# Kernel optimization log

Hardware: AMD Instinct MI355X
Metric: run time of the kernel (lower is better)

## Reference

```python
import jax, jax.numpy as jnp
import numpy as np

N_HEADS = 16
NEG_INF = -1e30


def apply_rope(x, cos, sin):
    # x: (B, T, H, D); cos/sin: (>=T, D//2)
    d = x.shape[-1]
    x1, x2 = x[..., : d // 2], x[..., d // 2 :]
    c = cos[: x.shape[1], :][None, :, None, :]  # (1, T, 1, D//2)
    s = sin[: x.shape[1], :][None, :, None, :]
    return jnp.concatenate([x1 * c - x2 * s, x2 * c + x1 * s], axis=-1)


def setup_inputs() -> dict:
    key = jax.random.key(0)
    k1, k2, k3, k4, k5 = jax.random.split(key, 5)
    B, T, D = 4, 2048, 2048
    hd = D // N_HEADS
    scale = 0.02
    return {
        "x": jax.random.normal(k1, (B, T, D), dtype=jnp.float32),
        "cos": jax.random.uniform(k2, (T, hd // 2), dtype=jnp.float32),
        "sin": jax.random.uniform(k3, (T, hd // 2), dtype=jnp.float32),
        "W_qkv": jax.random.normal(k4, (3 * D, D), dtype=jnp.float32) * scale,
        "W_out": jax.random.normal(k5, (D, D), dtype=jnp.float32) * scale,
    }


def reference(x, cos, sin, W_qkv, W_out):
    B, T, D = x.shape
    H = N_HEADS
    hd = D // H
    # fused QKV projection (torch Linear: y = x @ W.T)
    qkv = jnp.einsum("btd,ed->bte", x, W_qkv).reshape(B, T, 3, H, hd)
    q, k, v = qkv[:, :, 0], qkv[:, :, 1], qkv[:, :, 2]
    q = apply_rope(q, cos, sin)
    k = apply_rope(k, cos, sin)
    # causal SDPA, scale = 1/sqrt(head_dim)
    scores = jnp.einsum("bthd,bshd->bhts", q, k) / jnp.sqrt(jnp.asarray(hd, x.dtype))
    causal = jnp.tril(jnp.ones((T, T), dtype=bool))  # (T, T)
    scores = jnp.where(causal[None, None, :, :], scores, NEG_INF)
    attn = jax.nn.softmax(scores, axis=-1)
    out = jnp.einsum("bhts,bshd->bthd", attn, v).reshape(B, T, D)
    return jnp.einsum("btd,ed->bte", out, W_out)
```

## Files before the change

### kernel.cpp

```cpp
#include <hip/hip_runtime.h>
#include <hip/hip_bf16.h>
#include <stdint.h>

#define TDIM 2048
#define DDIM 2048
#define BDIM 4
#define HDIM 16
#define HD   128
#define E3   6144
#define KDIM 2048

typedef unsigned short u16;
typedef __bf16 bf16x8 __attribute__((ext_vector_type(8)));
typedef float  f32x4  __attribute__((ext_vector_type(4)));

__device__ __forceinline__ u16 f2bf(float f) {
  union { float f; uint32_t u; } x; x.f = f;
  uint32_t r = x.u + 0x7fffu + ((x.u >> 16) & 1u);
  return (u16)(r >> 16);
}
__device__ __forceinline__ float bf2f(u16 u) {
  union { uint32_t u; float f; } x; x.u = ((uint32_t)u) << 16;
  return x.f;
}

__device__ __forceinline__ void load16(const void* g, void* l) {
  __builtin_amdgcn_global_load_lds(
      (const __attribute__((address_space(1))) void*)g,
      (__attribute__((address_space(3))) void*)l, 16, 0, 0);
}

__global__ void cvt_kernel(const float* __restrict__ in, u16* __restrict__ out, int n) {
  int i = (blockIdx.x * 256 + threadIdx.x) * 4;
  if (i >= n) return;
  float4 v = *(const float4*)(in + i);
  ushort4 o;
  o.x = f2bf(v.x); o.y = f2bf(v.y); o.z = f2bf(v.z); o.w = f2bf(v.w);
  *(ushort4*)(out + i) = o;
}

template <int MODE>
__global__ __launch_bounds__(256) void gemm_bt(
    const u16* __restrict__ A, const u16* __restrict__ Bm,
    u16* __restrict__ qkOut, u16* __restrict__ vtOut, float* __restrict__ fOut) {
  __shared__ __align__(16) u16 As[128 * 64];
  __shared__ __align__(16) u16 Bs[128 * 64];
  const int tid = threadIdx.x;
  const int bn = blockIdx.x, bm = blockIdx.y;
  const int w = tid >> 6, lane = tid & 63;
  const int wr = w >> 1, wc = w & 1;
  const int lrow = lane & 15, lgrp = lane >> 4;

  f32x4 acc[4][4];
#pragma unroll
  for (int m = 0; m < 4; ++m)
#pragma unroll
    for (int n = 0; n < 4; ++n) {
      acc[m][n][0] = 0.f; acc[m][n][1] = 0.f; acc[m][n][2] = 0.f; acc[m][n][3] = 0.f;
    }

  const size_t aRow = (size_t)bm * 128;
  const size_t bRow = (size_t)bn * 128;

  for (int kt = 0; kt < KDIM / 64; ++kt) {
    const int kb = kt * 64;
#pragma unroll
    for (int is = 0; is < 4; ++is) {
      int u = is * 256 + tid;
      int r = u >> 3, blk = u & 7;
      load16(A + (aRow + r) * KDIM + kb + ((blk ^ (r & 7)) * 8),
             (char*)As + (size_t)u * 16);
    }
#pragma unroll
    for (int is = 0; is < 4; ++is) {
      int u = is * 256 + tid;
      int r = u >> 3, blk = u & 7;
      load16(Bm + (bRow + r) * KDIM + kb + ((blk ^ (r & 7)) * 8),
             (char*)Bs + (size_t)u * 16);
    }
    __syncthreads();

#pragma unroll
    for (int kk = 0; kk < 2; ++kk) {
      bf16x8 af[4], bfr[4];
#pragma unroll
      for (int m = 0; m < 4; ++m) {
        int row = wr * 64 + m * 16 + lrow;
        af[m] = *(const bf16x8*)(As + row * 64 + (((kk * 4 + lgrp) ^ (row & 7)) * 8));
      }
#pragma unroll
      for (int n = 0; n < 4; ++n) {
        int row = wc * 64 + n * 16 + lrow;
        bfr[n] = *(const bf16x8*)(Bs + row * 64 + (((kk * 4 + lgrp) ^ (row & 7)) * 8));
      }
#pragma unroll
      for (int m = 0; m < 4; ++m)
#pragma unroll
        for (int n = 0; n < 4; ++n)
          acc[m][n] = __builtin_amdgcn_mfma_f32_16x16x32_bf16(af[m], bfr[n], acc[m][n], 0, 0, 0);
    }
    __syncthreads();
  }

  const int col_base = bn * 128 + wc * 64;
  const int row_base = bm * 128 + wr * 64;
#pragma unroll
  for (int m = 0; m < 4; ++m) {
    int row0 = row_base + m * 16 + lgrp * 4;
#pragma unroll
    for (int n = 0; n < 4; ++n) {
      int col = col_base + n * 16 + lrow;
      if (MODE == 0) {
        if (bn < 32) {
#pragma unroll
          for (int i = 0; i < 4; ++i)
            qkOut[(size_t)(row0 + i) * 4096 + col] = f2bf(acc[m][n][i]);
        } else {
          int e = col - 4096;
          int hh = e >> 7, d = e & 127;
          int bb = row0 >> 11, t0 = row0 & 2047;
          ushort4 pk;
          pk.x = f2bf(acc[m][n][0]); pk.y = f2bf(acc[m][n][1]);
          pk.z = f2bf(acc[m][n][2]); pk.w = f2bf(acc[m][n][3]);
          *(ushort4*)(vtOut + ((size_t)(bb * HDIM + hh) * HD + d) * TDIM + t0) = pk;
        }
      } else {
#pragma unroll
        for (int i = 0; i < 4; ++i)
          fOut[(size_t)(row0 + i) * DDIM + col] = acc[m][n][i];
      }
    }
  }
}

__global__ void rope_kernel(u16* __restrict__ qkbuf,
                            const float* __restrict__ cosb, const float* __restrict__ sinb) {
  int gid = blockIdx.x * 256 + threadIdx.x;
  int d4 = gid & 15;
  int h = (gid >> 4) & 15;
  int which = (gid >> 8) & 1;
  int row = gid >> 9;
  int t = row & 2047;
  u16* base = qkbuf + (size_t)row * 4096 + which * 2048 + h * HD + d4 * 4;
  ushort4 u1 = *(ushort4*)base;
  ushort4 u2 = *(ushort4*)(base + 64);
  float4 c = *(const float4*)(cosb + (size_t)t * 64 + d4 * 4);
  float4 s = *(const float4*)(sinb + (size_t)t * 64 + d4 * 4);
  float x1[4] = {bf2f(u1.x), bf2f(u1.y), bf2f(u1.z), bf2f(u1.w)};
  float x2[4] = {bf2f(u2.x), bf2f(u2.y), bf2f(u2.z), bf2f(u2.w)};
  float cc[4] = {c.x, c.y, c.z, c.w};
  float ss[4] = {s.x, s.y, s.z, s.w};
  ushort4 o1, o2;
  o1.x = f2bf(x1[0]*cc[0] - x2[0]*ss[0]); o2.x = f2bf(x2[0]*cc[0] + x1[0]*ss[0]);
  o1.y = f2bf(x1[1]*cc[1] - x2[1]*ss[1]); o2.y = f2bf(x2[1]*cc[1] + x1[1]*ss[1]);
  o1.z = f2bf(x1[2]*cc[2] - x2[2]*ss[2]); o2.z = f2bf(x2[2]*cc[2] + x1[2]*ss[2]);
  o1.w = f2bf(x1[3]*cc[3] - x2[3]*ss[3]); o2.w = f2bf(x2[3]*cc[3] + x1[3]*ss[3]);
  *(ushort4*)base = o1;
  *(ushort4*)(base + 64) = o2;
}

__global__ __launch_bounds__(256) void attn_kernel(const u16* __restrict__ qkbuf,
                                                   const u16* __restrict__ vtbuf,
                                                   u16* __restrict__ ao) {
  __shared__ __align__(16) u16 Ks[64 * 128];
  __shared__ __align__(16) u16 Vs[128 * 64];
  __shared__ __align__(16) u16 Ps[4][16 * 64];
  const int tid = threadIdx.x;
  const int w = tid >> 6, lane = tid & 63;
  const int lrow = lane & 15, lgrp = lane >> 4;
  const int bh = blockIdx.y, b = bh >> 4, h = bh & 15;

  const u16* qbase = qkbuf + (size_t)b * TDIM * 4096 + h * HD;
  const u16* kbase = qbase + 2048;
  const u16* vbase = vtbuf + (size_t)(b * HDIM + h) * HD * TDIM;

  const float scale2 = 0.08838834764831845f * 1.4426950408889634f;

  for (int pass = 0; pass < 2; ++pass) {
    const int qt = pass == 0 ? (int)blockIdx.x : (31 - (int)blockIdx.x);
    const int q0 = qt * 64;

    const int qrow = q0 + w * 16 + lrow;
    bf16x8 qf[4];
#pragma unroll
    for (int kb = 0; kb < 4; ++kb)
      qf[kb] = *(const bf16x8*)(qbase + (size_t)qrow * 4096 + kb * 32 + lgrp * 8);

    f32x4 po[8];
#pragma unroll
    for (int n = 0; n < 8; ++n) { po[n][0]=0.f; po[n][1]=0.f; po[n][2]=0.f; po[n][3]=0.f; }
    float m_i[4], l_i[4];
#pragma unroll
    for (int i = 0; i < 4; ++i) { m_i[i] = -1e30f; l_i[i] = 0.f; }

    const int ntiles = qt + 1;
    for (int it = 0; it < ntiles; ++it) {
      const int kv0 = it * 64;
      __syncthreads();
#pragma unroll
      for (int is = 0; is < 4; ++is) {
        int u = is * 256 + tid;
        int r = u >> 4, blk = u & 15;
        load16(kbase + (size_t)(kv0 + r) * 4096 + ((blk ^ (r & 7)) * 8),
               (char*)Ks + (size_t)u * 16);
      }
#pragma unroll
      for (int is = 0; is < 4; ++is) {
        int u = is * 256 + tid;
        int r = u >> 3, blk = u & 7;
        load16(vbase + (size_t)r * TDIM + kv0 + ((blk ^ (r & 7)) * 8),
               (char*)Vs + (size_t)u * 16);
      }
      __syncthreads();

      f32x4 sacc[4];
#pragma unroll
      for (int c = 0; c < 4; ++c) {
        sacc[c][0]=0.f; sacc[c][1]=0.f; sacc[c][2]=0.f; sacc[c][3]=0.f;
        int row = c * 16 + lrow;
        int swz = row & 7;
#pragma unroll
        for (int kb = 0; kb < 4; ++kb) {
          bf16x8 kf = *(const bf16x8*)(Ks + row * 128 + ((kb * 4 + lgrp) ^ swz) * 8);
          sacc[c] = __builtin_amdgcn_mfma_f32_16x16x32_bf16(qf[kb], kf, sacc[c], 0, 0, 0);
        }
      }

      float sv[4][4];
      float mt[4] = {-1e30f, -1e30f, -1e30f, -1e30f};
      if (it == qt) {
#pragma unroll
        for (int c = 0; c < 4; ++c) {
          int kg = kv0 + c * 16 + lrow;
#pragma unroll
          for (int i = 0; i < 4; ++i) {
            int qg = q0 + w * 16 + lgrp * 4 + i;
            float v = sacc[c][i] * scale2;
            if (kg > qg) v = -1e30f;
            sv[c][i] = v;
            mt[i] = fmaxf(mt[i], v);
          }
        }
      } else {
#pragma unroll
        for (int c = 0; c < 4; ++c)
#pragma unroll
          for (int i = 0; i < 4; ++i) {
            float v = sacc[c][i] * scale2;
            sv[c][i] = v;
            mt[i] = fmaxf(mt[i], v);
          }
      }
#pragma unroll
      for (int msk = 1; msk < 16; msk <<= 1)
#pragma unroll
        for (int i = 0; i < 4; ++i) mt[i] = fmaxf(mt[i], __shfl_xor(mt[i], msk));

      bool grow = (mt[0] > m_i[0] + 11.f) || (mt[1] > m_i[1] + 11.f) ||
                  (mt[2] > m_i[2] + 11.f) || (mt[3] > m_i[3] + 11.f);
      if (__any(grow)) {
#pragma unroll
        for (int i = 0; i < 4; ++i) {
          float mn = fmaxf(m_i[i], mt[i]);
          float corr = exp2f(m_i[i] - mn);
          m_i[i] = mn;
          l_i[i] *= corr;
#pragma unroll
          for (int n = 0; n < 8; ++n) po[n][i] *= corr;
        }
      }

      float pv[4][4];
#pragma unroll
      for (int c = 0; c < 4; ++c)
#pragma unroll
        for (int i = 0; i < 4; ++i) {
          float p = exp2f(sv[c][i] - m_i[i]);
          pv[c][i] = p;
          l_i[i] += p;
        }

#pragma unroll
      for (int c = 0; c < 4; ++c) {
        int kcol = c * 16 + lrow;
#pragma unroll
        for (int i = 0; i < 4; ++i) {
          int prow = lgrp * 4 + i;
          Ps[w][prow * 64 + (((kcol >> 3) ^ (prow & 7)) * 8) + (kcol & 7)] = f2bf(pv[c][i]);
        }
      }
      bf16x8 pa[2];
#pragma unroll
      for (int kk = 0; kk < 2; ++kk)
        pa[kk] = *(const bf16x8*)(&Ps[w][lrow * 64 + (((kk * 4 + lgrp) ^ (lrow & 7)) * 8)]);
#pragma unroll
      for (int n = 0; n < 8; ++n) {
        int row = n * 16 + lrow;
        int swz = row & 7;
#pragma unroll
        for (int kk = 0; kk < 2; ++kk) {
          bf16x8 vf = *(const bf16x8*)(Vs + row * 64 + (((kk * 4 + lgrp) ^ swz) * 8));
          po[n] = __builtin_amdgcn_mfma_f32_16x16x32_bf16(pa[kk], vf, po[n], 0, 0, 0);
        }
      }
    }

#pragma unroll
    for (int msk = 1; msk < 16; msk <<= 1)
#pragma unroll
      for (int i = 0; i < 4; ++i) l_i[i] += __shfl_xor(l_i[i], msk);
#pragma unroll
    for (int n = 0; n < 8; ++n)
#pragma unroll
      for (int i = 0; i < 4; ++i) {
        int qg = q0 + w * 16 + lgrp * 4 + i;
        float v = po[n][i] / l_i[i];
        ao[(size_t)(b * TDIM + qg) * DDIM + h * HD + n * 16 + lrow] = f2bf(v);
      }
  }
}

extern "C" void kernel_launch(void* const* d_in, const int* in_sizes, int n_in,
                              void* d_out, int out_size, void* d_ws, size_t ws_size,
                              hipStream_t stream) {
  const float* x    = (const float*)d_in[0];
  const float* cosb = (const float*)d_in[1];
  const float* sinb = (const float*)d_in[2];
  const float* wqkv = (const float*)d_in[3];
  const float* wout = (const float*)d_in[4];
  float* out = (float*)d_out;
  char* ws = (char*)d_ws;
  u16* xb  = (u16*)(ws);
  u16* wqb = (u16*)(ws + 33554432);
  u16* wob = (u16*)(ws + 58720256);
  u16* qkb = (u16*)(ws + 67108864);
  u16* vtb = (u16*)(ws + 134217728);

  cvt_kernel<<<16384, 256, 0, stream>>>(x, xb, 16777216);
  cvt_kernel<<<12288, 256, 0, stream>>>(wqkv, wqb, 12582912);
  cvt_kernel<<<4096, 256, 0, stream>>>(wout, wob, 4194304);
  gemm_bt<0><<<dim3(48, 64), 256, 0, stream>>>(xb, wqb, qkb, vtb, nullptr);
  rope_kernel<<<16384, 256, 0, stream>>>(qkb, cosb, sinb);
  attn_kernel<<<dim3(16, 64), 256, 0, stream>>>(qkb, vtb, xb);
  gemm_bt<1><<<dim3(16, 64), 256, 0, stream>>>(xb, wob, nullptr, nullptr, out);
}
```

Measured before the change: 664.3 us.

## Double-buffer GEMM LDS tiles to overlap global loads with MFMA

The GEMM now uses two LDS buffers per operand and prefetches the next k-tile through global_load_lds while MFMAs run on the current tile. Each iteration ends with one vmcnt wait and one barrier instead of two syncthreads. Fragment loads are also split into two halves to interleave LDS reads with MFMA issue. LDS use doubles to 64 KB per block, which may lower occupancy. There is also a possible hazard: a buffer being prefetched into is only protected by the barrier at the end of the previous iteration.

```diff
diff --git a/kernel.cpp b/kernel.cpp
--- a/kernel.cpp
+++ b/kernel.cpp
@@ -43,8 +43,8 @@
 __global__ __launch_bounds__(256) void gemm_bt(
     const u16* __restrict__ A, const u16* __restrict__ Bm,
     u16* __restrict__ qkOut, u16* __restrict__ vtOut, float* __restrict__ fOut) {
-  __shared__ __align__(16) u16 As[128 * 64];
-  __shared__ __align__(16) u16 Bs[128 * 64];
+  __shared__ __align__(16) u16 As[2][128 * 64];
+  __shared__ __align__(16) u16 Bs[2][128 * 64];
   const int tid = threadIdx.x;
   const int bn = blockIdx.x, bm = blockIdx.y;
   const int w = tid >> 6, lane = tid & 63;
@@ -62,44 +62,71 @@
   const size_t aRow = (size_t)bm * 128;
   const size_t bRow = (size_t)bn * 128;
 
-  for (int kt = 0; kt < KDIM / 64; ++kt) {
+  auto STAGE = [&](int c, int kt) {
     const int kb = kt * 64;
 #pragma unroll
     for (int is = 0; is < 4; ++is) {
       int u = is * 256 + tid;
       int r = u >> 3, blk = u & 7;
       load16(A + (aRow + r) * KDIM + kb + ((blk ^ (r & 7)) * 8),
-             (char*)As + (size_t)u * 16);
-    }
-#pragma unroll
-    for (int is = 0; is < 4; ++is) {
-      int u = is * 256 + tid;
-      int r = u >> 3, blk = u & 7;
+             (char*)As[c] + (size_t)u * 16);
       load16(Bm + (bRow + r) * KDIM + kb + ((blk ^ (r & 7)) * 8),
-             (char*)Bs + (size_t)u * 16);
-    }
-    __syncthreads();
-
-#pragma unroll
-    for (int kk = 0; kk < 2; ++kk) {
-      bf16x8 af[4], bfr[4];
-#pragma unroll
-      for (int m = 0; m < 4; ++m) {
-        int row = wr * 64 + m * 16 + lrow;
-        af[m] = *(const bf16x8*)(As + row * 64 + (((kk * 4 + lgrp) ^ (row & 7)) * 8));
-      }
-#pragma unroll
-      for (int n = 0; n < 4; ++n) {
-        int row = wc * 64 + n * 16 + lrow;
-        bfr[n] = *(const bf16x8*)(Bs + row * 64 + (((kk * 4 + lgrp) ^ (row & 7)) * 8));
-      }
-#pragma unroll
-      for (int m = 0; m < 4; ++m)
-#pragma unroll
-        for (int n = 0; n < 4; ++n)
-          acc[m][n] = __builtin_amdgcn_mfma_f32_16x16x32_bf16(af[m], bfr[n], acc[m][n], 0, 0, 0);
-    }
-    __syncthreads();
+             (char*)Bs[c] + (size_t)u * 16);
+    }
+  };
+
+  STAGE(0, 0);
+  asm volatile("s_waitcnt vmcnt(0)" ::: "memory");
+  __builtin_amdgcn_s_barrier();
+  __builtin_amdgcn_sched_barrier(0);
+
+  for (int kt = 0; kt < KDIM / 64; ++kt) {
+    const int cur = kt & 1;
+    if (kt + 1 < KDIM / 64) STAGE(cur ^ 1, kt + 1);
+
+    bf16x8 bfr[4][2];
+#pragma unroll
+    for (int n = 0; n < 4; ++n) {
+      int row = wc * 64 + n * 16 + lrow;
+#pragma unroll
+      for (int k2 = 0; k2 < 2; ++k2)
+        bfr[n][k2] = *(const bf16x8*)(Bs[cur] + row * 64 + (((k2 * 4 + lgrp) ^ (row & 7)) * 8));
+    }
+    bf16x8 afA[2][2];
+#pragma unroll
+    for (int m = 0; m < 2; ++m) {
+      int row = wr * 64 + m * 16 + lrow;
+#pragma unroll
+      for (int k2 = 0; k2 < 2; ++k2)
+        afA[m][k2] = *(const bf16x8*)(As[cur] + row * 64 + (((k2 * 4 + lgrp) ^ (row & 7)) * 8));
+    }
+#pragma unroll
+    for (int m = 0; m < 2; ++m)
+#pragma unroll
+      for (int n = 0; n < 4; ++n)
+#pragma unroll
+        for (int k2 = 0; k2 < 2; ++k2)
+          acc[m][n] = __builtin_amdgcn_mfma_f32_16x16x32_bf16(afA[m][k2], bfr[n][k2], acc[m][n], 0, 0, 0);
+
+    bf16x8 afB[2][2];
+#pragma unroll
+    for (int m = 0; m < 2; ++m) {
+      int row = wr * 64 + (m + 2) * 16 + lrow;
+#pragma unroll
+      for (int k2 = 0; k2 < 2; ++k2)
+        afB[m][k2] = *(const bf16x8*)(As[cur] + row * 64 + (((k2 * 4 + lgrp) ^ (row & 7)) * 8));
+    }
+#pragma unroll
+    for (int m = 0; m < 2; ++m)
+#pragma unroll
+      for (int n = 0; n < 4; ++n)
+#pragma unroll
+        for (int k2 = 0; k2 < 2; ++k2)
+          acc[m + 2][n] = __builtin_amdgcn_mfma_f32_16x16x32_bf16(afB[m][k2], bfr[n][k2], acc[m + 2][n], 0, 0, 0);
+
+    asm volatile("s_waitcnt vmcnt(0)" ::: "memory");
+    __builtin_amdgcn_s_barrier();
+    __builtin_amdgcn_sched_barrier(0);
   }
 
   const int col_base = bn * 128 + wc * 64;
```

Result: slower. 683.8 us (+2.9%).
